# Kernel tuning notes

Hardware: AMD Instinct MI355X
Metric: run time of the kernel (lower is better)

The kernel has to match this reference:

```python
import jax, jax.numpy as jnp
import numpy as np

DEFAULT_MASK_VALUE = -0.7 * float(jnp.finfo(jnp.dtype('float32')).max)


def setup_inputs() -> dict:
    key = jax.random.key(0)
    k1, k2, k3, k4 = jax.random.split(key, 4)
    B, T, NQ, NKV, D = 2, 2048, 32, 8, 128
    query = jax.random.normal(k1, (B, T, NQ, D), dtype=jnp.float32)
    k = jax.random.normal(k2, (B, T, NKV, D), dtype=jnp.float32)
    v = jax.random.normal(k3, (B, T, NKV, D), dtype=jnp.float32)
    # packed-sequence segment ids: sorted small ints so segments are contiguous
    decoder_segment_ids = jnp.sort(jax.random.randint(k4, (B, T), 0, 4), axis=-1).astype(jnp.int32)
    return {"query": query, "key": k, "value": v, "decoder_segment_ids": decoder_segment_ids}


def _generate_attention_mask(q_seq_len, kv_seq_len, decoder_segment_ids):
    # segment mask: [b, 1, 1, t, s]
    seg = (decoder_segment_ids[:, :, None] == decoder_segment_ids[:, None, :])[:, None, None, :, :]
    # causal mask: [1, 1, 1, t, s]
    row = jax.lax.broadcasted_iota(jnp.int32, (q_seq_len, kv_seq_len), 0)
    col = jax.lax.broadcasted_iota(jnp.int32, (q_seq_len, kv_seq_len), 1)
    causal = (col <= row)[None, None, None, :, :]
    mask = jnp.logical_and(seg, causal)
    return jnp.where(mask, 0.0, DEFAULT_MASK_VALUE)


def _apply_mask_to_logits(logits, mask):
    return jnp.where(mask >= DEFAULT_MASK_VALUE * 0.5, logits, DEFAULT_MASK_VALUE)


def reference(query, key, value, decoder_segment_ids):
    b, t, n, d = query.shape
    n_kv = key.shape[2]
    g = n // n_kv  # query heads per kv head (GQA)
    q = query.reshape(b, t, n_kv, g, d)
    # qk product (no internal sqrt(d) scaling, matching AttentionOp.qk_product)
    logits = jnp.einsum('btkgd,bskd->bkgts', q, key)  # [b, n_kv, g, t, s]
    mask = _generate_attention_mask(t, key.shape[1], decoder_segment_ids)
    logits = _apply_mask_to_logits(logits, mask)
    weights = jax.nn.softmax(logits, axis=-1).astype(query.dtype)
    out = jnp.einsum('bkgts,bskd->btkgd', weights, value)
    return out.reshape(b, t, n, d)
```

## Files before the change

kernel.cpp:

```cpp
#include <hip/hip_runtime.h>


typedef __bf16 bf16x8 __attribute__((ext_vector_type(8)));
typedef __bf16 bf16x2 __attribute__((ext_vector_type(2)));
typedef _Float16 f16x8 __attribute__((ext_vector_type(8)));
typedef float f32x4 __attribute__((ext_vector_type(4)));
typedef unsigned int uint2v __attribute__((ext_vector_type(2)));

#define B_   2
#define T_   2048
#define NQ_  32
#define NKV_ 8
#define D_   128

#define MASKV (-3.0e38f)
#define LOG2E 1.44269504f
#define TILE_US 8192
#define WS_TILES_BYTES ((size_t)B_ * NKV_ * (T_ / 32) * TILE_US * 2)
#define WS_NEED (WS_TILES_BYTES + (size_t)B_ * T_ * 4)

static __device__ __forceinline__ unsigned short f2bf(float x) {
    union { float f; unsigned int u; } c; c.f = x;
    unsigned int r = c.u + 0x7fffu + ((c.u >> 16) & 1u);
    return (unsigned short)(r >> 16);
}

union U8  { unsigned short us[8]; bf16x8 v; };
union H8  { _Float16 h[8]; f16x8 v; };
union PKW { bf16x2 h; unsigned int u; };
union PA4 { unsigned int u[4]; bf16x8 v; };

static __device__ __forceinline__ void pl32swap(unsigned int& a, unsigned int& b) {
#if __has_builtin(__builtin_amdgcn_permlane32_swap)
    uint2v t = __builtin_amdgcn_permlane32_swap(a, b, false, false);
    a = t.x; b = t.y;
#else
    asm("s_nop 1\n\tv_permlane32_swap_b32 %0, %1" : "+v"(a), "+v"(b));
#endif
}
static __device__ __forceinline__ void pl16swap(unsigned int& a, unsigned int& b) {
#if __has_builtin(__builtin_amdgcn_permlane16_swap)
    uint2v t = __builtin_amdgcn_permlane16_swap(a, b, false, false);
    a = t.x; b = t.y;
#else
    asm("s_nop 1\n\tv_permlane16_swap_b32 %0, %1" : "+v"(a), "+v"(b));
#endif
}

__global__ __launch_bounds__(256)
void prep(const float* __restrict__ kg, const float* __restrict__ vg,
          unsigned short* __restrict__ ws)
{
    const int tid = threadIdx.x;
    const int st  = blockIdx.x;
    const int kvh = blockIdx.y;
    const int b   = blockIdx.z;
    unsigned short* base = ws + ((size_t)((b * NKV_ + kvh) * (T_ / 32) + st)) * TILE_US;

    #pragma unroll
    for (int it = 0; it < 2; ++it) {
        int task = tid + it * 256;
        int r = task >> 4, c16 = task & 15;
        const float* kp = kg + (((size_t)(b * T_ + st * 32 + r)) * NKV_ + kvh) * D_ + c16 * 8;
        H8 hu;
        #pragma unroll
        for (int j = 0; j < 8; ++j) hu.h[j] = (_Float16)kp[j];
        int c = c16 >> 2, qd = c16 & 3, hi = r >> 4, ln = r & 15;
        int slot = (c * 2 + hi) * 64 + qd * 16 + ln;
        *(f16x8*)(base + slot * 8) = hu.v;
    }
    #pragma unroll
    for (int it = 0; it < 2; ++it) {
        int task = tid + it * 256;
        int d = task & 127, sc = task >> 7;
        const float* vp = vg + (((size_t)(b * T_ + st * 32 + sc * 8)) * NKV_ + kvh) * D_ + d;
        U8 pk;
        #pragma unroll
        for (int j = 0; j < 8; ++j) pk.us[j] = f2bf(vp[j * (NKV_ * D_)]);
        int slot = (d >> 4) * 64 + sc * 16 + (d & 15);
        *(bf16x8*)(base + 4096 + slot * 8) = pk.v;
    }
}

__global__ __launch_bounds__(256)
void prep_sstart(const int* __restrict__ seg, int* __restrict__ sstart)
{
    int idx = blockIdx.x * 256 + threadIdx.x;
    int b = idx >> 11, t = idx & (T_ - 1);
    const int* sb = seg + b * T_;
    int target = sb[t];
    int lo = 0, hi = t;
    while (lo < hi) { int mid = (lo + hi) >> 1; if (sb[mid] < target) lo = mid + 1; else hi = mid; }
    sstart[idx] = lo;
}

__global__ __launch_bounds__(256)
void attn_fwd(const float* __restrict__ qg,
              const int* __restrict__ sstart,
              const unsigned short* __restrict__ ws,
              float* __restrict__ outg)
{
    const int tid  = threadIdx.x;
    const int wave = tid >> 6;
    const int lane = tid & 63;
    const int qd   = lane >> 4;
    const int ln   = lane & 15;

    const int i    = blockIdx.x;
    const int head = blockIdx.y;
    const int kvh  = head >> 2;
    const int b    = blockIdx.z;

    const unsigned short* wsbase =
        ws + ((size_t)((b * NKV_ + kvh) * (T_ / 32))) * TILE_US + lane * 8;

#define LOADKV(KB, VB, tl) do {                                                \
        const unsigned short* _tb = wsbase + (size_t)(tl) * TILE_US;           \
        _Pragma("unroll")                                                      \
        for (int _c = 0; _c < 4; ++_c) {                                       \
            KB[_c][0] = *(const f16x8*)(_tb + (_c * 2 + 0) * 512);             \
            KB[_c][1] = *(const f16x8*)(_tb + (_c * 2 + 1) * 512);             \
        }                                                                      \
        _Pragma("unroll")                                                      \
        for (int _s = 0; _s < 8; ++_s)                                         \
            VB[_s] = *(const bf16x8*)(_tb + 4096 + _s * 512);                  \
    } while (0)

#define COMPUTE(KB, VB, TL) do {                                               \
        const int _s0 = (TL) * 32;                                             \
        f32x4 S0 = {0.f,0.f,0.f,0.f}, S1 = {0.f,0.f,0.f,0.f};                  \
        __builtin_amdgcn_s_setprio(1);                                         \
        _Pragma("unroll")                                                      \
        for (int c = 0; c < 4; ++c) {                                          \
            S0 = __builtin_amdgcn_mfma_f32_16x16x32_f16(KB[c][0], qh[c], S0,0,0,0); \
            S1 = __builtin_amdgcn_mfma_f32_16x16x32_f16(KB[c][1], qh[c], S1,0,0,0); \
            S0 = __builtin_amdgcn_mfma_f32_16x16x32_f16(KB[c][0], ql[c], S0,0,0,0); \
            S1 = __builtin_amdgcn_mfma_f32_16x16x32_f16(KB[c][1], ql[c], S1,0,0,0); \
        }                                                                      \
        __builtin_amdgcn_s_setprio(0);                                         \
        float p0[4], p1[4];                                                    \
        if (_s0 >= wave_rs_max && _s0 + 31 <= wave_row_min) {                  \
            _Pragma("unroll")                                                  \
            for (int r = 0; r < 4; ++r) {                                      \
                p0[r] = exp2f(S0[r]);                                          \
                p1[r] = exp2f(S1[r]);                                          \
            }                                                                  \
        } else {                                                               \
            _Pragma("unroll")                                                  \
            for (int r = 0; r < 4; ++r) {                                      \
                int kv0 = _s0 + qd * 4 + r;                                    \
                int kv1 = kv0 + 16;                                            \
                float sv0 = (kv0 >= rs_l && kv0 <= trow_l) ? S0[r] : MASKV;    \
                float sv1 = (kv1 >= rs_l && kv1 <= trow_l) ? S1[r] : MASKV;    \
                p0[r] = exp2f(sv0);                                            \
                p1[r] = exp2f(sv1);                                            \
            }                                                                  \
        }                                                                      \
        l_lane += (p0[0] + p0[1]) + (p0[2] + p0[3])                            \
                + (p1[0] + p1[1]) + (p1[2] + p1[3]);                           \
        PKW c0, c1, c2, c3;                                                    \
        c0.h = (bf16x2){(__bf16)p0[0], (__bf16)p0[1]};                         \
        c1.h = (bf16x2){(__bf16)p0[2], (__bf16)p0[3]};                         \
        c2.h = (bf16x2){(__bf16)p1[0], (__bf16)p1[1]};                         \
        c3.h = (bf16x2){(__bf16)p1[2], (__bf16)p1[3]};                         \
        unsigned int w0 = c0.u, w1 = c1.u, w2 = c2.u, w3 = c3.u;               \
        pl32swap(w0, w2); pl32swap(w1, w3);                                    \
        pl16swap(w0, w2); pl16swap(w1, w3);                                    \
        PA4 pw; pw.u[0] = w0; pw.u[1] = w1; pw.u[2] = w2; pw.u[3] = w3;        \
        bf16x8 pa = pw.v;                                                      \
        __builtin_amdgcn_s_setprio(1);                                         \
        _Pragma("unroll")                                                      \
        for (int sub = 0; sub < 8; ++sub)                                      \
            O[sub] = __builtin_amdgcn_mfma_f32_16x16x32_bf16(pa, VB[sub], O[sub],0,0,0); \
        __builtin_amdgcn_s_setprio(0);                                         \
    } while (0)

    for (int phase = 0; phase < 2; ++phase) {
        const int t0 = (phase == 0 ? (2 * (int)gridDim.x - 1 - i) : i) * 64;

        f16x8 qh[4], ql[4];
        {
            const float* qrow =
                qg + (((size_t)(b * T_ + (t0 + wave * 16 + ln)) * NQ_) + head) * D_;
            #pragma unroll
            for (int c = 0; c < 4; ++c) {
                float4 a  = *(const float4*)(qrow + c * 32 + qd * 8);
                float4 b2 = *(const float4*)(qrow + c * 32 + qd * 8 + 4);
                float xs[8] = {a.x, a.y, a.z, a.w, b2.x, b2.y, b2.z, b2.w};
                H8 hu, lu;
                #pragma unroll
                for (int j = 0; j < 8; ++j) {
                    float x = xs[j] * LOG2E;
                    _Float16 h = (_Float16)x;
                    hu.h[j] = h;
                    lu.h[j] = (_Float16)(x - (float)h);
                }
                qh[c] = hu.v; ql[c] = lu.v;
            }
        }

        const int trow_l = t0 + wave * 16 + ln;
        const int rs_l   = sstart[b * T_ + trow_l];
        int wave_rs_max = rs_l;
        wave_rs_max = max(wave_rs_max, __shfl_xor(wave_rs_max, 1));
        wave_rs_max = max(wave_rs_max, __shfl_xor(wave_rs_max, 2));
        wave_rs_max = max(wave_rs_max, __shfl_xor(wave_rs_max, 4));
        wave_rs_max = max(wave_rs_max, __shfl_xor(wave_rs_max, 8));
        const int wave_row_min = t0 + wave * 16;

        const int tile0   = sstart[b * T_ + t0] >> 5;
        const int n_tiles = t0 / 32 + 2;

        f32x4 O[8];
        #pragma unroll
        for (int k = 0; k < 8; ++k) O[k] = (f32x4){0.f, 0.f, 0.f, 0.f};
        float l_lane = 0.f;

        f16x8  kA[4][2], kB_[4][2];
        bf16x8 vA[8], vB_[8];

        int t = tile0;
        LOADKV(kA, vA, t);
        while (t + 1 < n_tiles) {
            LOADKV(kB_, vB_, t + 1);
            COMPUTE(kA, vA, t);
            if (t + 2 < n_tiles) LOADKV(kA, vA, t + 2);
            COMPUTE(kB_, vB_, t + 1);
            t += 2;
        }
        if (t < n_tiles) COMPUTE(kA, vA, t);

        float l = l_lane;
        l += __shfl_xor(l, 16);
        l += __shfl_xor(l, 32);
        const float invl = 1.0f / l;
        int trow[4];
        float inv[4];
        #pragma unroll
        for (int r = 0; r < 4; ++r) {
            trow[r] = t0 + wave * 16 + qd * 4 + r;
            inv[r]  = __shfl(invl, qd * 4 + r);
        }
        #pragma unroll
        for (int sub = 0; sub < 8; ++sub) {
            #pragma unroll
            for (int r = 0; r < 4; ++r) {
                outg[(((size_t)(b * T_ + trow[r]) * NQ_) + head) * D_ + sub * 16 + ln] =
                    O[sub][r] * inv[r];
            }
        }
    }

#undef LOADKV
#undef COMPUTE
}

#define KSTR 136
#define VSTR 40
#define PSTR 40
static __device__ __forceinline__ float bf2f(unsigned short h) {
    union { unsigned int u; float f; } c; c.u = (unsigned int)h << 16; return c.f;
}
__global__ __launch_bounds__(256)
void attn_fwd_fb(const float* __restrict__ qg,
                 const float* __restrict__ kg,
                 const float* __restrict__ vg,
                 const int* __restrict__ seg,
                 float* __restrict__ outg)
{
    __shared__ unsigned short sKh[32 * KSTR];
    __shared__ unsigned short sKl[32 * KSTR];
    __shared__ unsigned short sVt[128 * VSTR];
    __shared__ unsigned short sP[4][16 * PSTR];

    const int tid  = threadIdx.x;
    const int wave = tid >> 6;
    const int lane = tid & 63;
    const int qd   = lane >> 4;
    const int ln   = lane & 15;
    const int t0   = ((int)gridDim.x - 1 - (int)blockIdx.x) * 64;
    const int head = blockIdx.y;
    const int kvh  = head >> 2;
    const int b    = blockIdx.z;

    bf16x8 qh[4], ql[4];
    {
        const float* qrow =
            qg + (((size_t)(b * T_ + (t0 + wave * 16 + ln)) * NQ_) + head) * D_;
        #pragma unroll
        for (int c = 0; c < 4; ++c) {
            float4 a  = *(const float4*)(qrow + c * 32 + qd * 8);
            float4 b2 = *(const float4*)(qrow + c * 32 + qd * 8 + 4);
            float xs[8] = {a.x, a.y, a.z, a.w, b2.x, b2.y, b2.z, b2.w};
            U8 hu, lu;
            #pragma unroll
            for (int j = 0; j < 8; ++j) {
                unsigned short h = f2bf(xs[j]);
                hu.us[j] = h;
                lu.us[j] = f2bf(xs[j] - bf2f(h));
            }
            qh[c] = hu.v; ql[c] = lu.v;
        }
    }
    const int* sb = seg + (size_t)b * T_;
    int qseg[4];
    #pragma unroll
    for (int r = 0; r < 4; ++r) qseg[r] = sb[t0 + wave * 16 + qd * 4 + r];
    int tile0;
    {
        int target = sb[t0];
        int lo = 0, hi = t0;
        while (lo < hi) { int mid = (lo + hi) >> 1; if (sb[mid] < target) lo = mid + 1; else hi = mid; }
        tile0 = lo >> 5;
    }
    f32x4 O[8];
    #pragma unroll
    for (int i = 0; i < 8; ++i) O[i] = (f32x4){0.f, 0.f, 0.f, 0.f};
    float m_prev[4], l_lane[4];
    #pragma unroll
    for (int r = 0; r < 4; ++r) { m_prev[r] = MASKV; l_lane[r] = 0.f; }
    const int n_tiles = t0 / 32 + 2;

    for (int tile = tile0; tile < n_tiles; ++tile) {
        const int s0 = tile * 32;
        __syncthreads();
        #pragma unroll
        for (int it = 0; it < 2; ++it) {
            int task = tid + it * 256;
            int r = task >> 4, d = (task & 15) * 8;
            const float* kp = kg + (((size_t)(b * T_ + s0 + r) * NKV_) + kvh) * D_ + d;
            float4 a  = *(const float4*)(kp);
            float4 b2 = *(const float4*)(kp + 4);
            float xs[8] = {a.x, a.y, a.z, a.w, b2.x, b2.y, b2.z, b2.w};
            U8 hu, lu;
            #pragma unroll
            for (int j = 0; j < 8; ++j) {
                unsigned short h = f2bf(xs[j]);
                hu.us[j] = h;
                lu.us[j] = f2bf(xs[j] - bf2f(h));
            }
            *(bf16x8*)(sKh + r * KSTR + d) = hu.v;
            *(bf16x8*)(sKl + r * KSTR + d) = lu.v;
        }
        #pragma unroll
        for (int it = 0; it < 2; ++it) {
            int task = tid + it * 256;
            int d = task & 127, sg = task >> 7;
            const float* vp = vg + (((size_t)(b * T_ + s0 + sg * 8) * NKV_) + kvh) * D_ + d;
            U8 pk;
            #pragma unroll
            for (int j = 0; j < 8; ++j) pk.us[j] = f2bf(vp[j * (NKV_ * D_)]);
            *(bf16x8*)(sVt + d * VSTR + sg * 8) = pk.v;
        }
        __syncthreads();

        f32x4 S0 = {0.f,0.f,0.f,0.f}, S1 = {0.f,0.f,0.f,0.f};
        #pragma unroll
        for (int c = 0; c < 4; ++c) {
            bf16x8 kh0 = *(const bf16x8*)(sKh + ln * KSTR + c * 32 + qd * 8);
            bf16x8 kh1 = *(const bf16x8*)(sKh + (16 + ln) * KSTR + c * 32 + qd * 8);
            bf16x8 kl0 = *(const bf16x8*)(sKl + ln * KSTR + c * 32 + qd * 8);
            bf16x8 kl1 = *(const bf16x8*)(sKl + (16 + ln) * KSTR + c * 32 + qd * 8);
            S0 = __builtin_amdgcn_mfma_f32_16x16x32_bf16(qh[c], kh0, S0, 0, 0, 0);
            S1 = __builtin_amdgcn_mfma_f32_16x16x32_bf16(qh[c], kh1, S1, 0, 0, 0);
            S0 = __builtin_amdgcn_mfma_f32_16x16x32_bf16(qh[c], kl0, S0, 0, 0, 0);
            S1 = __builtin_amdgcn_mfma_f32_16x16x32_bf16(qh[c], kl1, S1, 0, 0, 0);
            S0 = __builtin_amdgcn_mfma_f32_16x16x32_bf16(ql[c], kh0, S0, 0, 0, 0);
            S1 = __builtin_amdgcn_mfma_f32_16x16x32_bf16(ql[c], kh1, S1, 0, 0, 0);
        }
        const int ks0 = sb[s0 + ln];
        const int ks1 = sb[s0 + 16 + ln];
        float p0[4], p1[4], alpha[4];
        #pragma unroll
        for (int r = 0; r < 4; ++r) {
            const int trow = t0 + wave * 16 + qd * 4 + r;
            float s0v = ((s0 + ln <= trow) && (ks0 == qseg[r])) ? S0[r] : MASKV;
            float s1v = ((s0 + 16 + ln <= trow) && (ks1 == qseg[r])) ? S1[r] : MASKV;
            float mx = fmaxf(s0v, s1v);
            mx = fmaxf(mx, __shfl_xor(mx, 1));
            mx = fmaxf(mx, __shfl_xor(mx, 2));
            mx = fmaxf(mx, __shfl_xor(mx, 4));
            mx = fmaxf(mx, __shfl_xor(mx, 8));
            const float mn = fmaxf(m_prev[r], mx);
            alpha[r] = __expf(m_prev[r] - mn);
            p0[r] = __expf(s0v - mn);
            p1[r] = __expf(s1v - mn);
            l_lane[r] = alpha[r] * l_lane[r] + p0[r] + p1[r];
            m_prev[r] = mn;
        }
        #pragma unroll
        for (int i = 0; i < 8; ++i) {
            O[i][0] *= alpha[0]; O[i][1] *= alpha[1];
            O[i][2] *= alpha[2]; O[i][3] *= alpha[3];
        }
        {
            unsigned short* pw = sP[wave] + (qd * 4) * PSTR + ln;
            #pragma unroll
            for (int r = 0; r < 4; ++r) {
                pw[r * PSTR]      = f2bf(p0[r]);
                pw[r * PSTR + 16] = f2bf(p1[r]);
            }
        }
        asm volatile("s_waitcnt lgkmcnt(0)" ::: "memory");
        bf16x8 pa = *(const bf16x8*)(sP[wave] + ln * PSTR + qd * 8);
        #pragma unroll
        for (int sub = 0; sub < 8; ++sub) {
            bf16x8 bv = *(const bf16x8*)(sVt + (sub * 16 + ln) * VSTR + qd * 8);
            O[sub] = __builtin_amdgcn_mfma_f32_16x16x32_bf16(pa, bv, O[sub], 0, 0, 0);
        }
    }
    float inv[4];
    #pragma unroll
    for (int r = 0; r < 4; ++r) {
        float l = l_lane[r];
        l += __shfl_xor(l, 1);
        l += __shfl_xor(l, 2);
        l += __shfl_xor(l, 4);
        l += __shfl_xor(l, 8);
        inv[r] = 1.0f / l;
    }
    #pragma unroll
    for (int sub = 0; sub < 8; ++sub) {
        #pragma unroll
        for (int r = 0; r < 4; ++r) {
            const int trow = t0 + wave * 16 + qd * 4 + r;
            outg[(((size_t)(b * T_ + trow) * NQ_) + head) * D_ + sub * 16 + ln] =
                O[sub][r] * inv[r];
        }
    }
}

extern "C" void kernel_launch(void* const* d_in, const int* in_sizes, int n_in,
                              void* d_out, int out_size, void* d_ws, size_t ws_size,
                              hipStream_t stream) {
    const float* q  = (const float*)d_in[0];
    const float* k  = (const float*)d_in[1];
    const float* v  = (const float*)d_in[2];
    const int*   sg = (const int*)d_in[3];
    float*       o  = (float*)d_out;
    if (ws_size >= WS_NEED) {
        unsigned short* ws = (unsigned short*)d_ws;
        int* sstart = (int*)((char*)d_ws + WS_TILES_BYTES);
        prep<<<dim3(T_ / 32, NKV_, B_), dim3(256), 0, stream>>>(k, v, ws);
        prep_sstart<<<dim3(B_ * T_ / 256), dim3(256), 0, stream>>>(sg, sstart);
        attn_fwd<<<dim3(T_ / 128, NQ_, B_), dim3(256), 0, stream>>>(q, sstart, ws, o);
    } else {
        attn_fwd_fb<<<dim3(T_ / 64, NQ_, B_), dim3(256), 0, stream>>>(q, k, v, sg, o);
    }
}
```

Measured before the change: 224.3 us.

## Use single-wave blocks with 16-row query chunks and head-major grid ordering

The attention kernel now launches one 64-thread wave per block, each handling a 16-row query chunk per phase instead of four waves sharing a 64-row block. Head becomes the fastest grid dimension, so the four query heads sharing a KV head are scheduled close together for L2 reuse. Per-wave tile bounds are tightened so each wave only walks the KV tiles its own rows need, removing causal over-iteration and improving load balance. In exchange there are many more small blocks and the waves in a former block no longer share anything.

```diff
diff --git a/kernel.cpp b/kernel.cpp
--- a/kernel.cpp
+++ b/kernel.cpp
@@ -94,20 +94,18 @@
     sstart[idx] = lo;
 }
 
-__global__ __launch_bounds__(256)
+__global__ __launch_bounds__(64)
 void attn_fwd(const float* __restrict__ qg,
               const int* __restrict__ sstart,
               const unsigned short* __restrict__ ws,
               float* __restrict__ outg)
 {
-    const int tid  = threadIdx.x;
-    const int wave = tid >> 6;
-    const int lane = tid & 63;
+    const int lane = threadIdx.x & 63;
     const int qd   = lane >> 4;
     const int ln   = lane & 15;
 
-    const int i    = blockIdx.x;
-    const int head = blockIdx.y;
+    const int head = blockIdx.x;
+    const int j    = blockIdx.y;
     const int kvh  = head >> 2;
     const int b    = blockIdx.z;
 
@@ -176,12 +174,13 @@
     } while (0)
 
     for (int phase = 0; phase < 2; ++phase) {
-        const int t0 = (phase == 0 ? (2 * (int)gridDim.x - 1 - i) : i) * 64;
+        const int chunk = (phase == 0) ? (2 * (int)gridDim.y - 1 - j) : j;
+        const int t0 = chunk * 16;
 
         f16x8 qh[4], ql[4];
         {
             const float* qrow =
-                qg + (((size_t)(b * T_ + (t0 + wave * 16 + ln)) * NQ_) + head) * D_;
+                qg + (((size_t)(b * T_ + (t0 + ln)) * NQ_) + head) * D_;
             #pragma unroll
             for (int c = 0; c < 4; ++c) {
                 float4 a  = *(const float4*)(qrow + c * 32 + qd * 8);
@@ -189,27 +188,23 @@
                 float xs[8] = {a.x, a.y, a.z, a.w, b2.x, b2.y, b2.z, b2.w};
                 H8 hu, lu;
                 #pragma unroll
-                for (int j = 0; j < 8; ++j) {
-                    float x = xs[j] * LOG2E;
+                for (int jj = 0; jj < 8; ++jj) {
+                    float x = xs[jj] * LOG2E;
                     _Float16 h = (_Float16)x;
-                    hu.h[j] = h;
-                    lu.h[j] = (_Float16)(x - (float)h);
+                    hu.h[jj] = h;
+                    lu.h[jj] = (_Float16)(x - (float)h);
                 }
                 qh[c] = hu.v; ql[c] = lu.v;
             }
         }
 
-        const int trow_l = t0 + wave * 16 + ln;
+        const int trow_l = t0 + ln;
         const int rs_l   = sstart[b * T_ + trow_l];
-        int wave_rs_max = rs_l;
-        wave_rs_max = max(wave_rs_max, __shfl_xor(wave_rs_max, 1));
-        wave_rs_max = max(wave_rs_max, __shfl_xor(wave_rs_max, 2));
-        wave_rs_max = max(wave_rs_max, __shfl_xor(wave_rs_max, 4));
-        wave_rs_max = max(wave_rs_max, __shfl_xor(wave_rs_max, 8));
-        const int wave_row_min = t0 + wave * 16;
+        const int wave_rs_max  = sstart[b * T_ + t0 + 15];
+        const int wave_row_min = t0;
 
         const int tile0   = sstart[b * T_ + t0] >> 5;
-        const int n_tiles = t0 / 32 + 2;
+        const int n_tiles = ((t0 + 15) >> 5) + 1;
 
         f32x4 O[8];
         #pragma unroll
@@ -238,7 +233,7 @@
         float inv[4];
         #pragma unroll
         for (int r = 0; r < 4; ++r) {
-            trow[r] = t0 + wave * 16 + qd * 4 + r;
+            trow[r] = t0 + qd * 4 + r;
             inv[r]  = __shfl(invl, qd * 4 + r);
         }
         #pragma unroll
@@ -443,7 +438,7 @@
         int* sstart = (int*)((char*)d_ws + WS_TILES_BYTES);
         prep<<<dim3(T_ / 32, NKV_, B_), dim3(256), 0, stream>>>(k, v, ws);
         prep_sstart<<<dim3(B_ * T_ / 256), dim3(256), 0, stream>>>(sg, sstart);
-        attn_fwd<<<dim3(T_ / 128, NQ_, B_), dim3(256), 0, stream>>>(q, sstart, ws, o);
+        attn_fwd<<<dim3(NQ_, T_ / 32, B_), dim3(64), 0, stream>>>(q, sstart, ws, o);
     } else {
         attn_fwd_fb<<<dim3(T_ / 64, NQ_, B_), dim3(256), 0, stream>>>(q, k, v, sg, o);
     }
```

Result: faster. 198.6 us (-11.5%).
